# Performance work log

Hardware: AMD Instinct MI355X
Metric: run time of the kernel (lower is better)

Reference implementation:

```python
import jax, jax.numpy as jnp
import numpy as np

B, H, P, L = 8, 128, 128, 4096


def _cplx(x):
    # view_as_complex: (..., 2) float -> complex
    return x[..., 0] + 1j * x[..., 1]


def setup_inputs() -> dict:
    key = jax.random.key(0)
    ks = jax.random.split(key, 6)
    u = jax.random.normal(ks[0], (B, H, L), dtype=jnp.float32)
    C_ri = jax.random.normal(ks[1], (H, P, 2), dtype=jnp.float32)
    D_ri = jax.random.normal(ks[2], (H, H, 2), dtype=jnp.float32)
    # ContinuousStateReservoir: Re(Lambda) in [high_stability, low_stability] = [-1.0, -0.1]
    lam_re = jax.random.uniform(ks[3], (P,), minval=-1.0, maxval=-0.1, dtype=jnp.float32)
    lam_im = jax.random.normal(ks[4], (P,), dtype=jnp.float32) * np.float32(np.pi)
    Lam = lam_re + 1j * lam_im                      # continuous eigs
    Lam_bar = jnp.exp(Lam)                          # ZOH with Delta = 1
    B0 = jax.random.normal(ks[5], (P, H, 2), dtype=jnp.float32)
    Bc = _cplx(B0)
    B_bar = ((Lam_bar - 1.0) / Lam)[:, None] * Bc   # ZOH B_bar
    B_ri = jnp.stack([B_bar.real, B_bar.imag], axis=-1).astype(jnp.float32)
    Lambda_ri = jnp.stack([Lam_bar.real, Lam_bar.imag], axis=-1).astype(jnp.float32)
    return {"u": u, "C_ri": C_ri, "D_ri": D_ri, "B_ri": B_ri, "Lambda_ri": Lambda_ri}


def reference(u, C_ri, D_ri, B_ri, Lambda_ri):
    C = _cplx(C_ri)          # (H, P) complex
    D = _cplx(D_ri)          # (H, H)
    B_bar = _cplx(B_ri)      # (P, H)
    Lam_bar = _cplx(Lambda_ri)  # (P,)
    # torch.fft.rfftn defaults to ALL dims: complex FFT on (B,H), real FFT on L
    U_s = jnp.fft.rfftn(u)                                   # (B, H, Lf)
    s = 1j * (2.0 * jnp.pi * jnp.fft.rfftfreq(u.shape[-1]))  # (Lf,)
    mid = 1.0 / (s[None, :] - Lam_bar[:, None])              # (P, Lf) Cauchy kernel
    C_mid = jnp.einsum('hp,pl->hpl', C, mid)                 # (H, P, Lf)
    G = jnp.einsum('hpl,pq->hql', C_mid, B_bar)              # (H, H, Lf) transfer function
    Y_s = jnp.einsum('hql,bql->bhl', G, U_s) + jnp.einsum('hq,bql->bhl', D, U_s)
    y = jnp.fft.irfftn(Y_s)                                  # (B, H, L) real
    return jax.nn.gelu(y, approximate=False)
```

## Files before the change

kernel.cpp:

```cpp
#include <hip/hip_runtime.h>
#include <math.h>

#define Bn 8
#define Hn 128
#define Pn 128
#define Ln 4096
#define LF 2049
#define NROWS (Bn*Hn)
#define NT 16
#define NTILES 129
#define PLSZ 2048
#define WPLSZ 16384
#define TSCALE 64.0f

#define SKEW(a) ((a) + ((a) >> 4))
#define FBUF 2176

typedef _Float16 f16x8 __attribute__((ext_vector_type(8)));
typedef float f32x4 __attribute__((ext_vector_type(4)));

__device__ __forceinline__ void write3(_Float16* __restrict__ W, int idx,
                                       float vr, float vi) {
    W[0 * WPLSZ + idx] = (_Float16)vr;
    W[1 * WPLSZ + idx] = (_Float16)vi;
    W[2 * WPLSZ + idx] = (_Float16)(-vi);
}

__global__ void prep_ABE_k(const float* __restrict__ B_ri, const float* __restrict__ C_ri,
                           const float* __restrict__ D_ri,
                           _Float16* __restrict__ W1, _Float16* __restrict__ W2,
                           float2* __restrict__ E) {
    int bid = blockIdx.x;
    int idx = (bid & 63) * 256 + threadIdx.x;
    int rrow = idx >> 7, ccol = idx & 127;
    if (bid < 64) {
        float sr = 0.f, si = 0.f;
        for (int q = 0; q < 128; ++q) {
            float br = B_ri[(rrow * 128 + q) * 2 + 0];
            float bi = B_ri[(rrow * 128 + q) * 2 + 1];
            float ang = -3.14159265358979f * (float)((q * ccol) & 127) / 64.0f;
            float sw, cw; __sincosf(ang, &sw, &cw);
            sr += br * cw - bi * sw;
            si += br * sw + bi * cw;
        }
        write3(W1, idx, sr, si);
    } else if (bid < 128) {
        float sr = 0.f, si = 0.f;
        for (int h2 = 0; h2 < 128; ++h2) {
            float cr = C_ri[(h2 * 128 + ccol) * 2 + 0];
            float ci = C_ri[(h2 * 128 + ccol) * 2 + 1];
            float ang = 3.14159265358979f * (float)((rrow * h2) & 127) / 64.0f;
            float sw, cw; __sincosf(ang, &sw, &cw);
            sr += cr * cw - ci * sw;
            si += cr * sw + ci * cw;
        }
        write3(W2, idx, sr * (TSCALE / 128.0f), si * (TSCALE / 128.0f));
    } else {
        float sr = 0.f, si = 0.f;
        for (int c = 0; c < 128; ++c) {
            float dr = D_ri[(rrow * 128 + c) * 2 + 0];
            float di = D_ri[(rrow * 128 + c) * 2 + 1];
            float ang = -3.14159265358979f * (float)((c * ccol) & 127) / 64.0f;
            float sw, cw; __sincosf(ang, &sw, &cw);
            sr += dr * cw - di * sw;
            si += dr * sw + di * cw;
        }
        E[idx] = make_float2(sr, si);
    }
}

__global__ void prep_W3_k(const float2* __restrict__ E, _Float16* __restrict__ W3) {
    int idx = blockIdx.x * blockDim.x + threadIdx.x;
    int h = idx >> 7, q = idx & 127;
    float sr = 0.f, si = 0.f;
    for (int a = 0; a < 128; ++a) {
        float2 e = E[a * 128 + q];
        float ang = 3.14159265358979f * (float)((h * a) & 127) / 64.0f;
        float sw, cw; __sincosf(ang, &sw, &cw);
        sr += e.x * cw - e.y * sw;
        si += e.x * sw + e.y * cw;
    }
    write3(W3, idx, sr * (1.0f / 128.0f), si * (1.0f / 128.0f));
}

__device__ __forceinline__ float2 cadd2(float2 a, float2 b) { return make_float2(a.x + b.x, a.y + b.y); }
__device__ __forceinline__ float2 csub2(float2 a, float2 b) { return make_float2(a.x - b.x, a.y - b.y); }

template <int SIGN>
__device__ __forceinline__ void dft4(float2 a0, float2 a1, float2 a2, float2 a3,
                                     float2& y0, float2& y1, float2& y2, float2& y3) {
    float t0x = a0.x + a2.x, t0y = a0.y + a2.y;
    float t1x = a0.x - a2.x, t1y = a0.y - a2.y;
    float t2x = a1.x + a3.x, t2y = a1.y + a3.y;
    float t3x = a1.x - a3.x, t3y = a1.y - a3.y;
    y0 = make_float2(t0x + t2x, t0y + t2y);
    y2 = make_float2(t0x - t2x, t0y - t2y);
    y1 = make_float2(t1x - (float)SIGN * t3y, t1y + (float)SIGN * t3x);
    y3 = make_float2(t1x + (float)SIGN * t3y, t1y - (float)SIGN * t3x);
}

template <int SIGN>
__device__ __forceinline__ void fft2048(float2* bufA, float2* bufB) {
    const int tid = threadIdx.x;
    float2* src = bufA;
    float2* dst = bufB;
    #pragma unroll
    for (int stg = 0; stg < 3; ++stg) {
        const int ls = 3 * stg;
        const int k = tid;
        const int q = k & ((1 << ls) - 1);
        const int p = k >> ls;
        float2 a[8];
        #pragma unroll
        for (int u = 0; u < 8; ++u) a[u] = src[SKEW(k + (u << 8))];
        float2 A0, A1, A2, A3, B0, B1, B2, B3;
        dft4<SIGN>(a[0], a[2], a[4], a[6], A0, A1, A2, A3);
        dft4<SIGN>(a[1], a[3], a[5], a[7], B0, B1, B2, B3);
        const float c45 = 0.70710678118655f;
        float2 w1 = make_float2(c45 * (B1.x - (float)SIGN * B1.y), c45 * ((float)SIGN * B1.x + B1.y));
        float2 w2 = make_float2(-(float)SIGN * B2.y, (float)SIGN * B2.x);
        float2 w3 = make_float2(c45 * (-B3.x - (float)SIGN * B3.y), c45 * ((float)SIGN * B3.x - B3.y));
        float2 b[8];
        b[0] = cadd2(A0, B0);  b[4] = csub2(A0, B0);
        b[1] = cadd2(A1, w1);  b[5] = csub2(A1, w1);
        b[2] = cadd2(A2, w2);  b[6] = csub2(A2, w2);
        b[3] = cadd2(A3, w3);  b[7] = csub2(A3, w3);
        float ang = (float)SIGN * 6.28318530717959f * (float)p * (1.0f / (float)(2048 >> ls));
        #pragma unroll
        for (int j = 1; j < 8; ++j) {
            float sj, cj; __sincosf((float)j * ang, &sj, &cj);
            b[j] = make_float2(b[j].x * cj - b[j].y * sj, b[j].x * sj + b[j].y * cj);
        }
        const int base = q + (p << (ls + 3));
        #pragma unroll
        for (int j = 0; j < 8; ++j) dst[SKEW(base + (j << ls))] = b[j];
        __syncthreads();
        float2* t = src; src = dst; dst = t;
    }
    #pragma unroll
    for (int r = 0; r < 2; ++r) {
        int k = tid + (r << 8);
        float2 a0 = src[SKEW(k)];
        float2 a1 = src[SKEW(k + 512)];
        float2 a2 = src[SKEW(k + 1024)];
        float2 a3 = src[SKEW(k + 1536)];
        float2 y0, y1, y2, y3;
        dft4<SIGN>(a0, a1, a2, a3, y0, y1, y2, y3);
        dst[SKEW(k)] = y0;
        dst[SKEW(k + 512)] = y1;
        dst[SKEW(k + 1024)] = y2;
        dst[SKEW(k + 1536)] = y3;
    }
    __syncthreads();
}

__global__ __launch_bounds__(256, 4) void rfft_rows_k(const float* __restrict__ u,
                                                      float2* __restrict__ Uhat) {
    __shared__ __align__(16) float2 bufA[FBUF];
    __shared__ __align__(16) float2 bufB[FBUF];
    const int row = blockIdx.x;
    const int tid = threadIdx.x;
    const float2* up = (const float2*)(u + (size_t)row * Ln);
    for (int i = tid; i < 2048; i += 256) bufA[SKEW(i)] = up[i];
    __syncthreads();
    fft2048<-1>(bufA, bufB);
    float2* op = Uhat + (size_t)row * LF;
    for (int l = tid; l < 1025; l += 256) {
        float2 Zl = bufA[SKEW(l)];
        float2 Zm = bufA[SKEW((2048 - l) & 2047)];
        float2 Fe = make_float2(0.5f * (Zl.x + Zm.x), 0.5f * (Zl.y - Zm.y));
        float2 Dv = make_float2(0.5f * (Zl.x - Zm.x), 0.5f * (Zl.y + Zm.y));
        float2 Fo = make_float2(Dv.y, -Dv.x);
        float s, c; __sincosf(-3.14159265358979f * (float)l / 2048.0f, &s, &c);
        float2 TF = make_float2(Fo.x * c - Fo.y * s, Fo.x * s + Fo.y * c);
        op[l] = make_float2(Fe.x + TF.x, Fe.y + TF.y);
        op[2048 - l] = make_float2(Fe.x - TF.x, -(Fe.y - TF.y));
    }
}

__global__ __launch_bounds__(256, 4) void irfft_gelu_k(const float2* __restrict__ Uhat,
                                                       float* __restrict__ out) {
    __shared__ __align__(16) float2 bufA[FBUF];
    __shared__ __align__(16) float2 bufB[FBUF];
    const int row = blockIdx.x;
    const int tid = threadIdx.x;
    const float2* wp = Uhat + (size_t)row * LF;
    for (int l = tid; l < 1025; l += 256) {
        float2 Ul = wp[l];
        float2 Um = wp[2048 - l];
        float2 Fe = make_float2(0.5f * (Ul.x + Um.x), 0.5f * (Ul.y - Um.y));
        float2 Dv = make_float2(0.5f * (Ul.x - Um.x), 0.5f * (Ul.y + Um.y));
        float s, c; __sincosf(3.14159265358979f * (float)l / 2048.0f, &s, &c);
        float2 Fo = make_float2(Dv.x * c - Dv.y * s, Dv.x * s + Dv.y * c);
        bufA[SKEW(l)] = make_float2(Fe.x - Fo.y, Fe.y + Fo.x);
        if (l >= 1 && l <= 1023)
            bufA[SKEW(2048 - l)] = make_float2(Fe.x + Fo.y, Fo.x - Fe.y);
    }
    __syncthreads();
    fft2048<1>(bufA, bufB);
    float2* op = (float2*)(out + (size_t)row * Ln);
    for (int n = tid; n < 2048; n += 256) {
        float2 z = bufA[SKEW(n)];
        float y0 = z.x * (1.0f / 2048.0f);
        float y1 = z.y * (1.0f / 2048.0f);
        op[n] = make_float2(0.5f * y0 * (1.0f + erff(y0 * 0.70710678118655f)),
                            0.5f * y1 * (1.0f + erff(y1 * 0.70710678118655f)));
    }
}

__device__ __forceinline__ f32x4 mfma16h(f16x8 a, f16x8 b, f32x4 c) {
    return __builtin_amdgcn_mfma_f32_16x16x32_f16(a, b, c, 0, 0, 0);
}
__device__ __forceinline__ f16x8 read_frag(const _Float16* plane, int n, int k) {
    int ksw = k ^ ((n & 7) << 3);
    return *(const f16x8*)(plane + n * 128 + ksw);
}
__device__ __forceinline__ f16x8 aread(const _Float16* W, int pl, int m, int k) {
    return *(const f16x8*)(W + pl * WPLSZ + m * 128 + k);
}
__device__ __forceinline__ void cmfma4(f16x8 Wr, f16x8 Wi, f16x8 Wni,
                                       f16x8 br, f16x8 bi, f32x4& aR, f32x4& aI) {
    aR = mfma16h(Wr, br, aR);
    aR = mfma16h(Wni, bi, aR);
    aI = mfma16h(Wr, bi, aI);
    aI = mfma16h(Wi, br, aI);
}

__global__ __launch_bounds__(256, 4) void mixmm_k(float2* __restrict__ Uhat,
                                                  const _Float16* __restrict__ W1,
                                                  const _Float16* __restrict__ W2,
                                                  const _Float16* __restrict__ W3,
                                                  const float* __restrict__ Lam) {
    __shared__ __align__(16) _Float16 Up[2 * PLSZ];
    __shared__ __align__(16) _Float16 Tp[2 * PLSZ];
    __shared__ __align__(16) float2 Ustage[128 * NT];

    const int tid = threadIdx.x;
    const int b = blockIdx.x / NTILES;
    const int tile = blockIdx.x % NTILES;
    const int l0 = tile * NT;
    const int ncols = (LF - l0) < NT ? (LF - l0) : NT;

    for (int i = tid; i < 128 * NT; i += 256) {
        int h = i >> 4, n = i & 15;
        float2 v = make_float2(0.f, 0.f);
        if (n < ncols) v = Uhat[(size_t)(b * 128 + h) * LF + l0 + n];
        Ustage[h * NT + n] = v;
    }
    __syncthreads();

    {
        int n = tid & 15, kc = tid >> 4;
        f16x8 fr, fi;
        #pragma unroll
        for (int j = 0; j < 8; ++j) {
            float2 v = Ustage[(kc * 8 + j) * NT + n];
            fr[j] = (_Float16)v.x;
            fi[j] = (_Float16)v.y;
        }
        int ksw = (kc * 8) ^ ((n & 7) << 3);
        *(f16x8*)(Up + 0 * PLSZ + n * 128 + ksw) = fr;
        *(f16x8*)(Up + 1 * PLSZ + n * 128 + ksw) = fi;
    }
    __syncthreads();

    const int lane = tid & 63;
    const int w = tid >> 6;
    const int m15 = lane & 15;
    const int quad = lane >> 4;

    f32x4 aR[2], aI[2];
    #pragma unroll
    for (int s = 0; s < 2; ++s) { aR[s] = (f32x4)0.f; aI[s] = (f32x4)0.f; }

    #pragma unroll
    for (int kb = 0; kb < 4; ++kb) {
        int k = kb * 32 + quad * 8;
        f16x8 br = read_frag(Up + 0 * PLSZ, m15, k);
        f16x8 bi = read_frag(Up + 1 * PLSZ, m15, k);
        #pragma unroll
        for (int s = 0; s < 2; ++s) {
            int m = w * 32 + s * 16 + m15;
            cmfma4(aread(W1, 0, m, k), aread(W1, 1, m, k), aread(W1, 2, m, k),
                   br, bi, aR[s], aI[s]);
        }
    }

    #pragma unroll
    for (int s = 0; s < 2; ++s) {
        #pragma unroll
        for (int reg = 0; reg < 4; ++reg) {
            int p = w * 32 + s * 16 + quad * 4 + reg;
            float2 lamv = ((const float2*)Lam)[p];
            float dr = -lamv.x;
            int n = m15;
            int l = l0 + n;
            float di = 3.14159265358979f * (float)l / 2048.0f - lamv.y;
            float inv = (1.0f / TSCALE) / (dr * dr + di * di);
            float xr = aR[s][reg], xi = aI[s][reg];
            float tr = (xr * dr + xi * di) * inv;
            float ti = (xi * dr - xr * di) * inv;
            int off = n * 128 + (p ^ ((n & 7) << 3));
            Tp[0 * PLSZ + off] = (_Float16)tr;
            Tp[1 * PLSZ + off] = (_Float16)ti;
        }
    }
    __syncthreads();

    #pragma unroll
    for (int s = 0; s < 2; ++s) { aR[s] = (f32x4)0.f; aI[s] = (f32x4)0.f; }

    #pragma unroll
    for (int kb = 0; kb < 4; ++kb) {
        int k = kb * 32 + quad * 8;
        f16x8 tr = read_frag(Tp + 0 * PLSZ, m15, k);
        f16x8 ti = read_frag(Tp + 1 * PLSZ, m15, k);
        f16x8 ur = read_frag(Up + 0 * PLSZ, m15, k);
        f16x8 ui = read_frag(Up + 1 * PLSZ, m15, k);
        #pragma unroll
        for (int s = 0; s < 2; ++s) {
            int m = w * 32 + s * 16 + m15;
            cmfma4(aread(W2, 0, m, k), aread(W2, 1, m, k), aread(W2, 2, m, k),
                   tr, ti, aR[s], aI[s]);
            cmfma4(aread(W3, 0, m, k), aread(W3, 1, m, k), aread(W3, 2, m, k),
                   ur, ui, aR[s], aI[s]);
        }
    }

    #pragma unroll
    for (int s = 0; s < 2; ++s) {
        int n = m15;
        if (n < ncols) {
            #pragma unroll
            for (int reg = 0; reg < 4; ++reg) {
                int m = w * 32 + s * 16 + quad * 4 + reg;
                Uhat[(size_t)(b * 128 + m) * LF + l0 + n] = make_float2(aR[s][reg], aI[s][reg]);
            }
        }
    }
}

extern "C" void kernel_launch(void* const* d_in, const int* in_sizes, int n_in,
                              void* d_out, int out_size, void* d_ws, size_t ws_size,
                              hipStream_t stream) {
    const float* u    = (const float*)d_in[0];
    const float* C_ri = (const float*)d_in[1];
    const float* D_ri = (const float*)d_in[2];
    const float* B_ri = (const float*)d_in[3];
    const float* Lam  = (const float*)d_in[4];
    float* out = (float*)d_out;

    float2* Uhat = (float2*)d_ws;
    _Float16* W1 = (_Float16*)(Uhat + (size_t)NROWS * LF);
    _Float16* W2 = W1 + 3 * WPLSZ;
    _Float16* W3 = W2 + 3 * WPLSZ;
    float2* Em = (float2*)(W3 + 3 * WPLSZ);

    prep_ABE_k<<<192, 256, 0, stream>>>(B_ri, C_ri, D_ri, W1, W2, Em);
    prep_W3_k<<<64, 256, 0, stream>>>(Em, W3);

    rfft_rows_k<<<NROWS, 256, 0, stream>>>(u, Uhat);
    mixmm_k<<<Bn * NTILES, 256, 0, stream>>>(Uhat, W1, W2, W3, Lam);
    irfft_gelu_k<<<NROWS, 256, 0, stream>>>(Uhat, out);
}
```

Measured before the change: 171.9 us.

## Widen mix tiles, drop negated-imag weight plane, vectorize FFT IO, recur twiddles

The frequency-mix kernel now processes 32 frequency columns per block instead of 16, halving the number of blocks and the weight fragment reloads per column. The weights are stored without a negated-imaginary plane; a separate accumulator holds Wi*Bi and is subtracted at the end. The staging buffer in shared memory is removed in favour of direct per-thread loads. FFT twiddles inside the radix-8 stage are computed by complex recurrence from one sincos instead of seven. Row loads and GELU stores use float4 vectors. The trade-offs are more accumulator registers and slightly less accurate twiddles.

```diff
diff --git a/kernel.cpp b/kernel.cpp
--- a/kernel.cpp
+++ b/kernel.cpp
@@ -7,9 +7,9 @@
 #define Ln 4096
 #define LF 2049
 #define NROWS (Bn*Hn)
-#define NT 16
-#define NTILES 129
-#define PLSZ 2048
+#define NT 32
+#define NTILES 65
+#define PLSZ 4096
 #define WPLSZ 16384
 #define TSCALE 64.0f
 
@@ -19,11 +19,10 @@
 typedef _Float16 f16x8 __attribute__((ext_vector_type(8)));
 typedef float f32x4 __attribute__((ext_vector_type(4)));
 
-__device__ __forceinline__ void write3(_Float16* __restrict__ W, int idx,
+__device__ __forceinline__ void write2(_Float16* __restrict__ W, int idx,
                                        float vr, float vi) {
     W[0 * WPLSZ + idx] = (_Float16)vr;
     W[1 * WPLSZ + idx] = (_Float16)vi;
-    W[2 * WPLSZ + idx] = (_Float16)(-vi);
 }
 
 __global__ void prep_ABE_k(const float* __restrict__ B_ri, const float* __restrict__ C_ri,
@@ -43,7 +42,7 @@
             sr += br * cw - bi * sw;
             si += br * sw + bi * cw;
         }
-        write3(W1, idx, sr, si);
+        write2(W1, idx, sr, si);
     } else if (bid < 128) {
         float sr = 0.f, si = 0.f;
         for (int h2 = 0; h2 < 128; ++h2) {
@@ -54,7 +53,7 @@
             sr += cr * cw - ci * sw;
             si += cr * sw + ci * cw;
         }
-        write3(W2, idx, sr * (TSCALE / 128.0f), si * (TSCALE / 128.0f));
+        write2(W2, idx, sr * (TSCALE / 128.0f), si * (TSCALE / 128.0f));
     } else {
         float sr = 0.f, si = 0.f;
         for (int c = 0; c < 128; ++c) {
@@ -80,7 +79,7 @@
         sr += e.x * cw - e.y * sw;
         si += e.x * sw + e.y * cw;
     }
-    write3(W3, idx, sr * (1.0f / 128.0f), si * (1.0f / 128.0f));
+    write2(W3, idx, sr * (1.0f / 128.0f), si * (1.0f / 128.0f));
 }
 
 __device__ __forceinline__ float2 cadd2(float2 a, float2 b) { return make_float2(a.x + b.x, a.y + b.y); }
@@ -126,10 +125,14 @@
         b[2] = cadd2(A2, w2);  b[6] = csub2(A2, w2);
         b[3] = cadd2(A3, w3);  b[7] = csub2(A3, w3);
         float ang = (float)SIGN * 6.28318530717959f * (float)p * (1.0f / (float)(2048 >> ls));
+        float s1, c1; __sincosf(ang, &s1, &c1);
+        float cp = 1.f, sp = 0.f;
         #pragma unroll
         for (int j = 1; j < 8; ++j) {
-            float sj, cj; __sincosf((float)j * ang, &sj, &cj);
-            b[j] = make_float2(b[j].x * cj - b[j].y * sj, b[j].x * sj + b[j].y * cj);
+            float cn = cp * c1 - sp * s1;
+            float sn = cp * s1 + sp * c1;
+            cp = cn; sp = sn;
+            b[j] = make_float2(b[j].x * cp - b[j].y * sp, b[j].x * sp + b[j].y * cp);
         }
         const int base = q + (p << (ls + 3));
         #pragma unroll
@@ -160,8 +163,14 @@
     __shared__ __align__(16) float2 bufB[FBUF];
     const int row = blockIdx.x;
     const int tid = threadIdx.x;
-    const float2* up = (const float2*)(u + (size_t)row * Ln);
-    for (int i = tid; i < 2048; i += 256) bufA[SKEW(i)] = up[i];
+    const float4* up4 = (const float4*)(u + (size_t)row * Ln);
+    #pragma unroll
+    for (int r = 0; r < 4; ++r) {
+        float4 v = up4[tid + (r << 8)];
+        int i = 2 * (tid + (r << 8));
+        bufA[SKEW(i)] = make_float2(v.x, v.y);
+        bufA[SKEW(i + 1)] = make_float2(v.z, v.w);
+    }
     __syncthreads();
     fft2048<-1>(bufA, bufB);
     float2* op = Uhat + (size_t)row * LF;
@@ -198,13 +207,21 @@
     }
     __syncthreads();
     fft2048<1>(bufA, bufB);
-    float2* op = (float2*)(out + (size_t)row * Ln);
-    for (int n = tid; n < 2048; n += 256) {
-        float2 z = bufA[SKEW(n)];
-        float y0 = z.x * (1.0f / 2048.0f);
-        float y1 = z.y * (1.0f / 2048.0f);
-        op[n] = make_float2(0.5f * y0 * (1.0f + erff(y0 * 0.70710678118655f)),
-                            0.5f * y1 * (1.0f + erff(y1 * 0.70710678118655f)));
+    float4* op4 = (float4*)(out + (size_t)row * Ln);
+    #pragma unroll
+    for (int r = 0; r < 4; ++r) {
+        int n = 2 * (tid + (r << 8));
+        float2 z0 = bufA[SKEW(n)];
+        float2 z1 = bufA[SKEW(n + 1)];
+        float y0 = z0.x * (1.0f / 2048.0f);
+        float y1 = z0.y * (1.0f / 2048.0f);
+        float y2 = z1.x * (1.0f / 2048.0f);
+        float y3 = z1.y * (1.0f / 2048.0f);
+        op4[tid + (r << 8)] = make_float4(
+            0.5f * y0 * (1.0f + erff(y0 * 0.70710678118655f)),
+            0.5f * y1 * (1.0f + erff(y1 * 0.70710678118655f)),
+            0.5f * y2 * (1.0f + erff(y2 * 0.70710678118655f)),
+            0.5f * y3 * (1.0f + erff(y3 * 0.70710678118655f)));
     }
 }
 
@@ -217,13 +234,6 @@
 }
 __device__ __forceinline__ f16x8 aread(const _Float16* W, int pl, int m, int k) {
     return *(const f16x8*)(W + pl * WPLSZ + m * 128 + k);
-}
-__device__ __forceinline__ void cmfma4(f16x8 Wr, f16x8 Wi, f16x8 Wni,
-                                       f16x8 br, f16x8 bi, f32x4& aR, f32x4& aI) {
-    aR = mfma16h(Wr, br, aR);
-    aR = mfma16h(Wni, bi, aR);
-    aI = mfma16h(Wr, bi, aI);
-    aI = mfma16h(Wi, br, aI);
 }
 
 __global__ __launch_bounds__(256, 4) void mixmm_k(float2* __restrict__ Uhat,
@@ -233,7 +243,6 @@
                                                   const float* __restrict__ Lam) {
     __shared__ __align__(16) _Float16 Up[2 * PLSZ];
     __shared__ __align__(16) _Float16 Tp[2 * PLSZ];
-    __shared__ __align__(16) float2 Ustage[128 * NT];
 
     const int tid = threadIdx.x;
     const int b = blockIdx.x / NTILES;
@@ -241,26 +250,27 @@
     const int l0 = tile * NT;
     const int ncols = (LF - l0) < NT ? (LF - l0) : NT;
 
-    for (int i = tid; i < 128 * NT; i += 256) {
-        int h = i >> 4, n = i & 15;
-        float2 v = make_float2(0.f, 0.f);
-        if (n < ncols) v = Uhat[(size_t)(b * 128 + h) * LF + l0 + n];
-        Ustage[h * NT + n] = v;
-    }
-    __syncthreads();
-
     {
-        int n = tid & 15, kc = tid >> 4;
-        f16x8 fr, fi;
-        #pragma unroll
-        for (int j = 0; j < 8; ++j) {
-            float2 v = Ustage[(kc * 8 + j) * NT + n];
-            fr[j] = (_Float16)v.x;
-            fi[j] = (_Float16)v.y;
-        }
-        int ksw = (kc * 8) ^ ((n & 7) << 3);
-        *(f16x8*)(Up + 0 * PLSZ + n * 128 + ksw) = fr;
-        *(f16x8*)(Up + 1 * PLSZ + n * 128 + ksw) = fi;
+        int n = tid & 31, kc = tid >> 5;
+        float2 v[16];
+        #pragma unroll
+        for (int j = 0; j < 16; ++j) {
+            int h = kc * 16 + j;
+            v[j] = (n < ncols) ? Uhat[(size_t)(b * 128 + h) * LF + l0 + n]
+                               : make_float2(0.f, 0.f);
+        }
+        #pragma unroll
+        for (int jc = 0; jc < 2; ++jc) {
+            f16x8 fr, fi;
+            #pragma unroll
+            for (int j = 0; j < 8; ++j) {
+                fr[j] = (_Float16)v[jc * 8 + j].x;
+                fi[j] = (_Float16)v[jc * 8 + j].y;
+            }
+            int ksw = (kc * 16 + jc * 8) ^ ((n & 7) << 3);
+            *(f16x8*)(Up + 0 * PLSZ + n * 128 + ksw) = fr;
+            *(f16x8*)(Up + 1 * PLSZ + n * 128 + ksw) = fi;
+        }
     }
     __syncthreads();
 
@@ -269,21 +279,39 @@
     const int m15 = lane & 15;
     const int quad = lane >> 4;
 
-    f32x4 aR[2], aI[2];
-    #pragma unroll
-    for (int s = 0; s < 2; ++s) { aR[s] = (f32x4)0.f; aI[s] = (f32x4)0.f; }
+    f32x4 accR[2][2], accM[2][2], accI[2][2];
+    #pragma unroll
+    for (int s = 0; s < 2; ++s)
+        #pragma unroll
+        for (int t = 0; t < 2; ++t) {
+            accR[s][t] = (f32x4)0.f; accM[s][t] = (f32x4)0.f; accI[s][t] = (f32x4)0.f;
+        }
 
     #pragma unroll
     for (int kb = 0; kb < 4; ++kb) {
         int k = kb * 32 + quad * 8;
-        f16x8 br = read_frag(Up + 0 * PLSZ, m15, k);
-        f16x8 bi = read_frag(Up + 1 * PLSZ, m15, k);
+        f16x8 wr[2], wi[2];
         #pragma unroll
         for (int s = 0; s < 2; ++s) {
             int m = w * 32 + s * 16 + m15;
-            cmfma4(aread(W1, 0, m, k), aread(W1, 1, m, k), aread(W1, 2, m, k),
-                   br, bi, aR[s], aI[s]);
-        }
+            wr[s] = aread(W1, 0, m, k);
+            wi[s] = aread(W1, 1, m, k);
+        }
+        f16x8 br[2], bi[2];
+        #pragma unroll
+        for (int t = 0; t < 2; ++t) {
+            br[t] = read_frag(Up + 0 * PLSZ, t * 16 + m15, k);
+            bi[t] = read_frag(Up + 1 * PLSZ, t * 16 + m15, k);
+        }
+        #pragma unroll
+        for (int s = 0; s < 2; ++s)
+            #pragma unroll
+            for (int t = 0; t < 2; ++t) {
+                accR[s][t] = mfma16h(wr[s], br[t], accR[s][t]);
+                accM[s][t] = mfma16h(wi[s], bi[t], accM[s][t]);
+                accI[s][t] = mfma16h(wr[s], bi[t], accI[s][t]);
+                accI[s][t] = mfma16h(wi[s], br[t], accI[s][t]);
+            }
     }
 
     #pragma unroll
@@ -293,48 +321,96 @@
             int p = w * 32 + s * 16 + quad * 4 + reg;
             float2 lamv = ((const float2*)Lam)[p];
             float dr = -lamv.x;
-            int n = m15;
-            int l = l0 + n;
-            float di = 3.14159265358979f * (float)l / 2048.0f - lamv.y;
-            float inv = (1.0f / TSCALE) / (dr * dr + di * di);
-            float xr = aR[s][reg], xi = aI[s][reg];
-            float tr = (xr * dr + xi * di) * inv;
-            float ti = (xi * dr - xr * di) * inv;
-            int off = n * 128 + (p ^ ((n & 7) << 3));
-            Tp[0 * PLSZ + off] = (_Float16)tr;
-            Tp[1 * PLSZ + off] = (_Float16)ti;
+            #pragma unroll
+            for (int t = 0; t < 2; ++t) {
+                int n = t * 16 + m15;
+                int l = l0 + n;
+                float di = 3.14159265358979f * (float)l / 2048.0f - lamv.y;
+                float inv = (1.0f / TSCALE) / (dr * dr + di * di);
+                float xr = accR[s][t][reg] - accM[s][t][reg];
+                float xi = accI[s][t][reg];
+                float tr = (xr * dr + xi * di) * inv;
+                float ti = (xi * dr - xr * di) * inv;
+                int off = n * 128 + (p ^ ((n & 7) << 3));
+                Tp[0 * PLSZ + off] = (_Float16)tr;
+                Tp[1 * PLSZ + off] = (_Float16)ti;
+            }
         }
     }
     __syncthreads();
 
     #pragma unroll
-    for (int s = 0; s < 2; ++s) { aR[s] = (f32x4)0.f; aI[s] = (f32x4)0.f; }
+    for (int s = 0; s < 2; ++s)
+        #pragma unroll
+        for (int t = 0; t < 2; ++t) {
+            accR[s][t] = (f32x4)0.f; accM[s][t] = (f32x4)0.f; accI[s][t] = (f32x4)0.f;
+        }
 
     #pragma unroll
     for (int kb = 0; kb < 4; ++kb) {
         int k = kb * 32 + quad * 8;
-        f16x8 tr = read_frag(Tp + 0 * PLSZ, m15, k);
-        f16x8 ti = read_frag(Tp + 1 * PLSZ, m15, k);
-        f16x8 ur = read_frag(Up + 0 * PLSZ, m15, k);
-        f16x8 ui = read_frag(Up + 1 * PLSZ, m15, k);
-        #pragma unroll
-        for (int s = 0; s < 2; ++s) {
-            int m = w * 32 + s * 16 + m15;
-            cmfma4(aread(W2, 0, m, k), aread(W2, 1, m, k), aread(W2, 2, m, k),
-                   tr, ti, aR[s], aI[s]);
-            cmfma4(aread(W3, 0, m, k), aread(W3, 1, m, k), aread(W3, 2, m, k),
-                   ur, ui, aR[s], aI[s]);
+        {
+            f16x8 wr[2], wi[2];
+            #pragma unroll
+            for (int s = 0; s < 2; ++s) {
+                int m = w * 32 + s * 16 + m15;
+                wr[s] = aread(W2, 0, m, k);
+                wi[s] = aread(W2, 1, m, k);
+            }
+            f16x8 br[2], bi[2];
+            #pragma unroll
+            for (int t = 0; t < 2; ++t) {
+                br[t] = read_frag(Tp + 0 * PLSZ, t * 16 + m15, k);
+                bi[t] = read_frag(Tp + 1 * PLSZ, t * 16 + m15, k);
+            }
+            #pragma unroll
+            for (int s = 0; s < 2; ++s)
+                #pragma unroll
+                for (int t = 0; t < 2; ++t) {
+                    accR[s][t] = mfma16h(wr[s], br[t], accR[s][t]);
+                    accM[s][t] = mfma16h(wi[s], bi[t], accM[s][t]);
+                    accI[s][t] = mfma16h(wr[s], bi[t], accI[s][t]);
+                    accI[s][t] = mfma16h(wi[s], br[t], accI[s][t]);
+                }
+        }
+        {
+            f16x8 wr[2], wi[2];
+            #pragma unroll
+            for (int s = 0; s < 2; ++s) {
+                int m = w * 32 + s * 16 + m15;
+                wr[s] = aread(W3, 0, m, k);
+                wi[s] = aread(W3, 1, m, k);
+            }
+            f16x8 br[2], bi[2];
+            #pragma unroll
+            for (int t = 0; t < 2; ++t) {
+                br[t] = read_frag(Up + 0 * PLSZ, t * 16 + m15, k);
+                bi[t] = read_frag(Up + 1 * PLSZ, t * 16 + m15, k);
+            }
+            #pragma unroll
+            for (int s = 0; s < 2; ++s)
+                #pragma unroll
+                for (int t = 0; t < 2; ++t) {
+                    accR[s][t] = mfma16h(wr[s], br[t], accR[s][t]);
+                    accM[s][t] = mfma16h(wi[s], bi[t], accM[s][t]);
+                    accI[s][t] = mfma16h(wr[s], bi[t], accI[s][t]);
+                    accI[s][t] = mfma16h(wi[s], br[t], accI[s][t]);
+                }
         }
     }
 
     #pragma unroll
     for (int s = 0; s < 2; ++s) {
-        int n = m15;
-        if (n < ncols) {
-            #pragma unroll
-            for (int reg = 0; reg < 4; ++reg) {
-                int m = w * 32 + s * 16 + quad * 4 + reg;
-                Uhat[(size_t)(b * 128 + m) * LF + l0 + n] = make_float2(aR[s][reg], aI[s][reg]);
+        #pragma unroll
+        for (int t = 0; t < 2; ++t) {
+            int n = t * 16 + m15;
+            if (n < ncols) {
+                #pragma unroll
+                for (int reg = 0; reg < 4; ++reg) {
+                    int m = w * 32 + s * 16 + quad * 4 + reg;
+                    Uhat[(size_t)(b * 128 + m) * LF + l0 + n] =
+                        make_float2(accR[s][t][reg] - accM[s][t][reg], accI[s][t][reg]);
+                }
             }
         }
     }
@@ -352,9 +428,9 @@
 
     float2* Uhat = (float2*)d_ws;
     _Float16* W1 = (_Float16*)(Uhat + (size_t)NROWS * LF);
-    _Float16* W2 = W1 + 3 * WPLSZ;
-    _Float16* W3 = W2 + 3 * WPLSZ;
-    float2* Em = (float2*)(W3 + 3 * WPLSZ);
+    _Float16* W2 = W1 + 2 * WPLSZ;
+    _Float16* W3 = W2 + 2 * WPLSZ;
+    float2* Em = (float2*)(W3 + 2 * WPLSZ);
 
     prep_ABE_k<<<192, 256, 0, stream>>>(B_ri, C_ri, D_ri, W1, W2, Em);
     prep_W3_k<<<64, 256, 0, stream>>>(Em, W3);
```

After: 145.9 us. -15.1%, faster.
